# Kernel tuning notes

Measured on AMD Instinct MI355X. Metric: run time of the kernel, lower is better.

The kernel has to match this reference:

```python
import jax, jax.numpy as jnp
import numpy as np

D_MODEL, D_HEAD, N_HEADS, D_LATENT, D_ROPE = 2048, 128, 16, 512, 64
ROPE_BASE = 10000.0
SCALE = 1.0 / np.sqrt(D_HEAD + D_ROPE)


def _rope(x):
    # x: [B, H, T, d_rope]; GPT-NeoX style half-split rotary
    T, d = x.shape[-2], x.shape[-1]
    inv_freq = 1.0 / (ROPE_BASE ** (jnp.arange(0, d, 2, dtype=jnp.float32) / d))
    ang = jnp.arange(T, dtype=jnp.float32)[:, None] * inv_freq[None, :]  # [T, d/2]
    cos = jnp.concatenate([jnp.cos(ang), jnp.cos(ang)], axis=-1)  # [T, d]
    sin = jnp.concatenate([jnp.sin(ang), jnp.sin(ang)], axis=-1)
    x1, x2 = x[..., : d // 2], x[..., d // 2 :]
    rot = jnp.concatenate([-x2, x1], axis=-1)
    return x * cos + rot * sin


def setup_inputs() -> dict:
    key = jax.random.key(0)
    ks = jax.random.split(key, 8)
    B, T = 2, 2048
    s = 0.02
    inp = {
        "x": jax.random.normal(ks[0], (B, T, D_MODEL), jnp.float32),
        "w_q": jax.random.normal(ks[1], (D_MODEL, D_MODEL), jnp.float32) * s,
        "w_dkv": jax.random.normal(ks[2], (D_LATENT, D_MODEL), jnp.float32) * s,
        "w_ukv": jax.random.normal(ks[3], (2 * D_MODEL, D_LATENT), jnp.float32) * s,
        "w_o": jax.random.normal(ks[4], (D_MODEL, D_MODEL), jnp.float32) * s,
        "w_q_rot": jax.random.normal(ks[5], (N_HEADS * D_ROPE, D_MODEL), jnp.float32) * s,
        "w_k_rot": jax.random.normal(ks[6], (D_ROPE, D_MODEL), jnp.float32) * s,
        "mask": jnp.triu(jnp.ones((T, T), dtype=bool), 1),  # True = blocked (causal)
    }
    return inp


def reference(x, w_q, w_dkv, w_ukv, w_o, w_q_rot, w_k_rot, mask):
    B, T, _ = x.shape
    # content queries  [B, H, T, d_head]
    q = (x @ w_q.T).reshape(B, T, N_HEADS, D_HEAD).transpose(0, 2, 1, 3)
    # latent KV compression -> expansion
    dkv = x @ w_dkv.T                       # [B, T, d_latent]
    ukv = (dkv @ w_ukv.T).reshape(B, T, N_HEADS, 2 * D_HEAD).transpose(0, 2, 1, 3)
    k, v = ukv[..., :D_HEAD], ukv[..., D_HEAD:]
    # decoupled rope parts
    q_rot = (x @ w_q_rot.T).reshape(B, T, N_HEADS, D_ROPE).transpose(0, 2, 1, 3)
    k_rot = jnp.broadcast_to((x @ w_k_rot.T)[:, None, :, :], (B, N_HEADS, T, D_ROPE))
    q = jnp.concatenate([q, _rope(q_rot)], axis=-1)   # [B, H, T, d_head+d_rope]
    k = jnp.concatenate([k, _rope(k_rot)], axis=-1)
    # SDPA with True-means-blocked mask
    scores = jnp.einsum("bhqd,bhkd->bhqk", q, k) * SCALE
    scores = jnp.where(mask, -jnp.inf, scores)
    attn = jax.nn.softmax(scores, axis=-1)
    out = jnp.einsum("bhqk,bhkd->bhqd", attn, v)      # [B, H, T, d_head]
    out = out.transpose(0, 2, 1, 3).reshape(B, T, D_MODEL)
    return out @ w_o.T
```

## Files before the change

### kernel.cpp

```cpp
#include <hip/hip_runtime.h>
#include <hip/hip_bf16.h>
#include <math.h>

#define T_SEQ 2048
#define QSTR  3648

typedef __bf16 bf16x8 __attribute__((ext_vector_type(8)));
typedef float  f32x4  __attribute__((ext_vector_type(4)));
typedef float  f32x16 __attribute__((ext_vector_type(16)));
typedef unsigned int u32x4 __attribute__((ext_vector_type(4)));

#define GLOAD_LDS16(g, l) __builtin_amdgcn_global_load_lds( \
    (const __attribute__((address_space(1))) void*)(g),      \
    (__attribute__((address_space(3))) void*)(l), 16, 0, 0)

#define VMCNT(n) asm volatile("s_waitcnt vmcnt(" #n ")" ::: "memory")

static __device__ __forceinline__ unsigned cvtpk_bf16(float a, float b)
{
    unsigned r;
    asm("v_cvt_pk_bf16_f32 %0, %1, %2" : "=v"(r) : "v"(a), "v"(b));
    return r;
}

struct CastArgs {
    const float* s[7];
    __bf16*      d[7];
    unsigned     cum[8];
};

__global__ __launch_bounds__(256) void cast_all(CastArgs a)
{
    const unsigned blk = blockIdx.x;
    int idx = 0;
    #pragma unroll
    for (int i = 1; i < 7; i++) if (blk >= a.cum[i]) idx = i;
    const unsigned local = blk - a.cum[idx];
    const float* src = a.s[idx];
    __bf16* dst = a.d[idx];
    const int i = (int)(local * 256 + threadIdx.x) * 8;
    float4 va = *reinterpret_cast<const float4*>(src + i);
    float4 vb = *reinterpret_cast<const float4*>(src + i + 4);
    bf16x8 f;
    f[0] = (__bf16)va.x; f[1] = (__bf16)va.y; f[2] = (__bf16)va.z; f[3] = (__bf16)va.w;
    f[4] = (__bf16)vb.x; f[5] = (__bf16)vb.y; f[6] = (__bf16)vb.z; f[7] = (__bf16)vb.w;
    *reinterpret_cast<bf16x8*>(dst + i) = f;
}

__global__ __launch_bounds__(256) void rope_ip(__bf16* buf, int shift, int stride,
                                               int total)
{
    int gid = blockIdx.x * 256 + threadIdx.x;
    if (gid >= total) return;
    int row = gid >> shift;
    int rem = gid & ((1 << shift) - 1);
    int hb = rem >> 5, j = rem & 31;
    int t = row & (T_SEQ - 1);
    const float L2B = 0.4152410118609203f;
    float freq = exp2f(-L2B * (float)j);
    float sn, cs;
    __sincosf((float)t * freq, &sn, &cs);
    size_t base = (size_t)row * stride + hb * 64 + j;
    float v1 = (float)buf[base], v2 = (float)buf[base + 32];
    buf[base]      = (__bf16)(v1 * cs - v2 * sn);
    buf[base + 32] = (__bf16)(v2 * cs + v1 * sn);
}

__global__ __launch_bounds__(256) void prep_v(const __bf16* __restrict__ ukv,
                                              __bf16* __restrict__ vtt)
{
    __shared__ __align__(16) __bf16 Ls[64 * 136];
    const int tid = threadIdx.x;
    const int u = blockIdx.x, bh = blockIdx.y;
    const int b = bh >> 4, h = bh & 15;
    const size_t base = (size_t)b * T_SEQ + u * 64;
    #pragma unroll
    for (int p = 0; p < 4; p++) {
        int c = tid + 256 * p;
        int k = c >> 4, dv8 = (c & 15) * 8;
        *reinterpret_cast<bf16x8*>(Ls + k * 136 + dv8) =
            *reinterpret_cast<const bf16x8*>(ukv + (base + k) * 4096 + h * 256 + 128 + dv8);
    }
    __syncthreads();
    #pragma unroll
    for (int p = 0; p < 4; p++) {
        int c = tid + 256 * p;
        int dv = c >> 3, kb = c & 7;
        bf16x8 f;
        #pragma unroll
        for (int i = 0; i < 8; i++) f[i] = Ls[(kb * 8 + i) * 136 + dv];
        *reinterpret_cast<bf16x8*>(vtt + (((size_t)bh * 32 + u) * 128 + dv) * 64
                                   + ((kb ^ (dv & 7)) << 3)) = f;
    }
}

template <typename OutT>
__global__ __launch_bounds__(512, 2) void gemm_bt_256(const __bf16* __restrict__ A,
                                                      int lda,
                                                      const __bf16* __restrict__ B,
                                                      OutT* __restrict__ C,
                                                      int M, int N, int K)
{
    __shared__ __align__(16) __bf16 S[2 * 32768];
    const int tid  = threadIdx.x;
    const int lane = tid & 63;
    const int w    = tid >> 6;
    const int l15  = lane & 15, quad = lane >> 4;
    const int wm = w >> 2, wn = w & 3;
    const int m0 = blockIdx.y * 256, n0 = blockIdx.x * 256;
    const int NT = K >> 6;

    f32x4 acc[8][4] = {};
    bf16x8 af[4][2], bfr[2][2];

    auto stageA = [&](int T1, int h) {
        int d = T1 & 1;
        #pragma unroll
        for (int i = 0; i < 2; i++) {
            int c = i * 512 + tid;
            int lr = c >> 3, seg = c & 7;
            int g = ((lr >> 6) << 7) + h * 64 + (lr & 63);
            GLOAD_LDS16(A + (size_t)(m0 + g) * lda + T1 * 64 + ((seg ^ (lr & 7)) << 3),
                        S + d * 32768 + h * 8192 + c * 8);
        }
    };
    auto stageB = [&](int T1, int h) {
        int d = T1 & 1;
        #pragma unroll
        for (int i = 0; i < 2; i++) {
            int c = i * 512 + tid;
            int lr = c >> 3, seg = c & 7;
            int g = n0 + ((lr >> 5) << 6) + h * 32 + (lr & 31);
            if (g >= N) g = N - 1;
            GLOAD_LDS16(B + (size_t)g * K + T1 * 64 + ((seg ^ (lr & 7)) << 3),
                        S + d * 32768 + 16384 + h * 8192 + c * 8);
        }
    };

#define LOADA(d, mh) do {                                                      \
    const __bf16* Ah_ = S + (d) * 32768 + (mh) * 8192;                         \
    _Pragma("unroll")                                                          \
    for (int mi = 0; mi < 4; mi++) {                                           \
        int lr = wm * 64 + mi * 16 + l15;                                      \
        _Pragma("unroll")                                                      \
        for (int kk = 0; kk < 2; kk++)                                         \
            af[mi][kk] = *reinterpret_cast<const bf16x8*>(                     \
                Ah_ + lr * 64 + (((kk * 4 + quad) ^ (lr & 7)) << 3));          \
    }                                                                          \
} while (0)

#define LOADB(d, nh) do {                                                      \
    const __bf16* Bh_ = S + (d) * 32768 + 16384 + (nh) * 8192;                 \
    _Pragma("unroll")                                                          \
    for (int ni = 0; ni < 2; ni++) {                                           \
        int lr = wn * 32 + ni * 16 + l15;                                      \
        _Pragma("unroll")                                                      \
        for (int kk = 0; kk < 2; kk++)                                         \
            bfr[ni][kk] = *reinterpret_cast<const bf16x8*>(                    \
                Bh_ + lr * 64 + (((kk * 4 + quad) ^ (lr & 7)) << 3));          \
    }                                                                          \
} while (0)

#define SEAL() do {                                                            \
    __builtin_amdgcn_s_barrier();                                              \
    asm volatile("s_waitcnt lgkmcnt(0)" ::: "memory");                         \
    __builtin_amdgcn_sched_barrier(0);                                         \
} while (0)

#define MMA(mh, nh) do {                                                       \
    __builtin_amdgcn_s_setprio(1);                                             \
    _Pragma("unroll")                                                          \
    for (int mi = 0; mi < 4; mi++)                                             \
        _Pragma("unroll")                                                      \
        for (int ni = 0; ni < 2; ni++)                                         \
            _Pragma("unroll")                                                  \
            for (int kk = 0; kk < 2; kk++)                                     \
                acc[(mh) * 4 + mi][(nh) * 2 + ni] =                            \
                    __builtin_amdgcn_mfma_f32_16x16x32_bf16(                   \
                        af[mi][kk], bfr[ni][kk],                               \
                        acc[(mh) * 4 + mi][(nh) * 2 + ni], 0, 0, 0);           \
    __builtin_amdgcn_s_setprio(0);                                             \
} while (0)

    stageA(0, 0); stageB(0, 0); stageB(0, 1); stageA(0, 1);
    VMCNT(4);
    __builtin_amdgcn_s_barrier();

    for (int T = 0; T < NT - 1; T++) {
        const int d = T & 1;
        LOADA(d, 0); LOADB(d, 0); stageA(T + 1, 0); VMCNT(4); SEAL(); MMA(0, 0);
        LOADB(d, 1);              stageB(T + 1, 0); VMCNT(4); SEAL(); MMA(0, 1);
        LOADA(d, 1);              stageB(T + 1, 1);           SEAL(); MMA(1, 1);
        LOADB(d, 0);              stageA(T + 1, 1); VMCNT(4); SEAL(); MMA(1, 0);
    }
    {
        const int d = (NT - 1) & 1;
        LOADA(d, 0); LOADB(d, 0); VMCNT(2); SEAL(); MMA(0, 0);
        LOADB(d, 1);              VMCNT(0); SEAL(); MMA(0, 1);
        LOADA(d, 1);                        SEAL(); MMA(1, 1);
        LOADB(d, 0);                        SEAL(); MMA(1, 0);
    }
#undef LOADA
#undef LOADB
#undef SEAL
#undef MMA

    #pragma unroll
    for (int ai = 0; ai < 8; ai++) {
        #pragma unroll
        for (int bj = 0; bj < 4; bj++) {
            int col = n0 + wn * 64 + bj * 16 + l15;
            if (col < N) {
                #pragma unroll
                for (int r = 0; r < 4; r++) {
                    size_t row = m0 + wm * 128 + ai * 16 + quad * 4 + r;
                    C[row * (size_t)N + col] = (OutT)acc[ai][bj][r];
                }
            }
        }
    }
}

template <typename OutT>
__global__ __launch_bounds__(512) void gemm_bt_8ph(const __bf16* __restrict__ A,
                                                   int lda,
                                                   const __bf16* __restrict__ B,
                                                   OutT* __restrict__ C,
                                                   int M, int N, int K)
{
    __shared__ __align__(16) __bf16 S[2 * 24576];
    const int tid  = threadIdx.x;
    const int lane = tid & 63;
    const int w    = tid >> 6;
    const int l15  = lane & 15, quad = lane >> 4;
    const int wm = w >> 2, wn = w & 3;
    const int m0 = blockIdx.y * 128, n0 = blockIdx.x * 256;
    const int NT = K >> 6;

    f32x4 acc[4][4] = {};

    const int lrA = tid >> 3, segA = tid & 7;

    auto stageA = [&](int T1, int h) {
        int d = T1 & 1;
        int g = ((lrA >> 5) << 6) + h * 32 + (lrA & 31);
        GLOAD_LDS16(A + (size_t)(m0 + g) * lda + T1 * 64 + ((segA ^ (lrA & 7)) << 3),
                    S + d * 24576 + h * 4096 + tid * 8);
    };
    auto stageB = [&](int T1, int h) {
        int d = T1 & 1;
        #pragma unroll
        for (int i = 0; i < 2; i++) {
            int c = i * 512 + tid;
            int lr = c >> 3, seg = c & 7;
            int g = n0 + ((lr >> 5) << 6) + h * 32 + (lr & 31);
            if (g >= N) g = N - 1;
            GLOAD_LDS16(B + (size_t)g * K + T1 * 64 + ((seg ^ (lr & 7)) << 3),
                        S + d * 24576 + 8192 + h * 8192 + c * 8);
        }
    };

#define PHASE(d, mh, nh, STAGE, WAIT) do {                                     \
    const __bf16* Ah_ = S + (d) * 24576 + (mh) * 4096;                         \
    const __bf16* Bh_ = S + (d) * 24576 + 8192 + (nh) * 8192;                  \
    bf16x8 af[2][2], bfr[2][2];                                                \
    _Pragma("unroll")                                                          \
    for (int mr = 0; mr < 2; mr++) {                                           \
        int ar = wm * 32 + mr * 16 + l15;                                      \
        _Pragma("unroll")                                                      \
        for (int kk = 0; kk < 2; kk++)                                         \
            af[mr][kk] = *reinterpret_cast<const bf16x8*>(                     \
                Ah_ + ar * 64 + (((kk * 4 + quad) ^ (ar & 7)) << 3));          \
    }                                                                          \
    _Pragma("unroll")                                                          \
    for (int nr = 0; nr < 2; nr++) {                                           \
        int br = wn * 32 + nr * 16 + l15;                                      \
        _Pragma("unroll")                                                      \
        for (int kk = 0; kk < 2; kk++)                                         \
            bfr[nr][kk] = *reinterpret_cast<const bf16x8*>(                    \
                Bh_ + br * 64 + (((kk * 4 + quad) ^ (br & 7)) << 3));          \
    }                                                                          \
    STAGE;                                                                     \
    WAIT;                                                                      \
    __builtin_amdgcn_s_barrier();                                              \
    asm volatile("s_waitcnt lgkmcnt(0)" ::: "memory");                         \
    __builtin_amdgcn_sched_barrier(0);                                         \
    __builtin_amdgcn_s_setprio(1);                                             \
    _Pragma("unroll")                                                          \
    for (int mr = 0; mr < 2; mr++)                                             \
        _Pragma("unroll")                                                      \
        for (int nr = 0; nr < 2; nr++)                                         \
            _Pragma("unroll")                                                  \
            for (int kk = 0; kk < 2; kk++)                                     \
                acc[(mh) * 2 + mr][(nh) * 2 + nr] =                            \
                    __builtin_amdgcn_mfma_f32_16x16x32_bf16(                   \
                        af[mr][kk], bfr[nr][kk],                               \
                        acc[(mh) * 2 + mr][(nh) * 2 + nr], 0, 0, 0);           \
    __builtin_amdgcn_s_setprio(0);                                             \
} while (0)

    stageA(0, 0);
    stageB(0, 0);
    stageB(0, 1);
    stageA(0, 1);
    VMCNT(3);
    __builtin_amdgcn_s_barrier();

    for (int T = 0; T < NT - 1; T++) {
        const int d = T & 1;
        PHASE(d, 0, 0, stageA(T + 1, 0), VMCNT(2));
        PHASE(d, 0, 1, stageB(T + 1, 0), VMCNT(3));
        PHASE(d, 1, 0, stageB(T + 1, 1), (void)0);
        PHASE(d, 1, 1, stageA(T + 1, 1), VMCNT(3));
    }
    {
        const int d = (NT - 1) & 1;
        PHASE(d, 0, 0, (void)0, VMCNT(1));
        PHASE(d, 0, 1, (void)0, VMCNT(0));
        PHASE(d, 1, 0, (void)0, (void)0);
        PHASE(d, 1, 1, (void)0, (void)0);
    }
#undef PHASE

    #pragma unroll
    for (int ai = 0; ai < 4; ai++) {
        #pragma unroll
        for (int bj = 0; bj < 4; bj++) {
            int col = n0 + wn * 64 + bj * 16 + l15;
            if (col < N) {
                #pragma unroll
                for (int r = 0; r < 4; r++) {
                    size_t row = m0 + wm * 64 + ai * 16 + quad * 4 + r;
                    C[row * (size_t)N + col] = (OutT)acc[ai][bj][r];
                }
            }
        }
    }
}

__global__ __launch_bounds__(256, 2) void flash_mfma(
    const __bf16* __restrict__ qcat, const __bf16* __restrict__ ukv,
    const __bf16* __restrict__ vtt, __bf16* __restrict__ obuf)
{
    __shared__ __align__(16) __bf16 LDS[40960];

    const int tid  = threadIdx.x;
    const int w    = tid >> 6;
    const int lane = tid & 63;
    const int l31  = lane & 31;
    const int lh   = lane >> 5;
    const int l15  = lane & 15;
    const int quad = lane >> 4;
    const int gx = blockIdx.x, gy = blockIdx.y;
    int bh, qi;
    if (gy < 16) { bh = gy * 2;            qi = gx; }
    else         { bh = (gy - 16) * 2 + 1; qi = 15 - gx; }
    const int b = bh >> 4, h = bh & 15;
    const int q0 = qi * 128;
    const float SCALE = 0.07216878364870323f;
    const size_t urow = (size_t)b * T_SEQ;

    const int q = q0 + 32 * w + l31;
    bf16x8 qf[12];
    {
        const __bf16* qrow = qcat + (urow + q) * QSTR + h * 128;
        #pragma unroll
        for (int dk = 0; dk < 8; dk++)
            qf[dk] = *reinterpret_cast<const bf16x8*>(qrow + 16 * dk + 8 * lh);
        const __bf16* qrr = qcat + (urow + q) * QSTR + 2048 + h * 64;
        #pragma unroll
        for (int dk = 0; dk < 4; dk++)
            qf[8 + dk] = *reinterpret_cast<const bf16x8*>(qrr + 16 * dk + 8 * lh);
    }

    f32x16 o[4] = {};
    float m_i = -INFINITY, l_i = 0.f;

    const int nunits = 2 * qi + 2;

    auto stage = [&](int x) {
        const int d1 = x & 1;
        const size_t roff = urow + (size_t)64 * x;
        #pragma unroll
        for (int p = 0; p < 4; p++) {
            int c = tid + 256 * p;
            int row = c >> 4, seg = c & 15;
            GLOAD_LDS16(ukv + (roff + row) * 4096 + h * 256 + ((seg ^ (row & 7)) << 3),
                        LDS + d1 * 8192 + c * 8);
        }
        #pragma unroll
        for (int p = 0; p < 2; p++) {
            int c = tid + 256 * p;
            int row = c >> 3, seg = c & 7;
            GLOAD_LDS16(qcat + (roff + row) * QSTR + 3072 + ((seg ^ (row & 7)) << 3),
                        LDS + 16384 + d1 * 4096 + c * 8);
        }
        const __bf16* vsrc = vtt + ((size_t)bh * 32 + x) * 8192;
        #pragma unroll
        for (int p = 0; p < 4; p++) {
            int c = tid + 256 * p;
            GLOAD_LDS16(vsrc + c * 8, LDS + 24576 + d1 * 8192 + c * 8);
        }
    };

    stage(0);
    VMCNT(0);
    __builtin_amdgcn_s_barrier();

    for (int u = 0; u < nunits; u++) {
        if (u + 1 < nunits) { stage(u + 1); VMCNT(10); }
        else                { VMCNT(0); }
        __builtin_amdgcn_s_barrier();
        __builtin_amdgcn_sched_barrier(0);

        const int d1 = u & 1;
        const __bf16* KN = LDS + d1 * 8192;
        const __bf16* KR = LDS + 16384 + d1 * 4096;
        const __bf16* VT = LDS + 24576 + d1 * 8192;
        const int key = l31 & 7;

        f32x16 s2[2] = {};
        __builtin_amdgcn_s_setprio(1);
        #pragma unroll
        for (int t = 0; t < 2; t++) {
            const __bf16* kn = KN + (32 * t + l31) * 128;
            const __bf16* kr = KR + (32 * t + l31) * 64;
            #pragma unroll
            for (int dk = 0; dk < 8; dk++) {
                bf16x8 kf = *reinterpret_cast<const bf16x8*>(kn + (((2 * dk + lh) ^ key) << 3));
                s2[t] = __builtin_amdgcn_mfma_f32_32x32x16_bf16(kf, qf[dk], s2[t], 0, 0, 0);
            }
            #pragma unroll
            for (int dk = 0; dk < 4; dk++) {
                bf16x8 kf = *reinterpret_cast<const bf16x8*>(kr + (((2 * dk + lh) ^ key) << 3));
                s2[t] = __builtin_amdgcn_mfma_f32_32x32x16_bf16(kf, qf[8 + dk], s2[t], 0, 0, 0);
            }
        }
        __builtin_amdgcn_s_setprio(0);

        const int k0 = 64 * u;
        const bool domask = (u + 2 >= nunits);
        float rmax = -INFINITY;
        #pragma unroll
        for (int t = 0; t < 2; t++)
            #pragma unroll
            for (int g = 0; g < 16; g++) {
                float v = s2[t][g] * SCALE;
                if (domask) {
                    int kg = k0 + 32 * t + (g & 3) + 8 * (g >> 2) + 4 * lh;
                    if (kg > q) v = -INFINITY;
                }
                s2[t][g] = v;
                rmax = fmaxf(rmax, v);
            }
        rmax = fmaxf(rmax, __shfl_xor(rmax, 32, 64));
        const float mnew  = fmaxf(m_i, rmax);
        const float alpha = __expf(m_i - mnew);
        m_i = mnew;
        float part = 0.f;
        #pragma unroll
        for (int t = 0; t < 2; t++)
            #pragma unroll
            for (int g = 0; g < 16; g++) {
                float pv = __expf(s2[t][g] - mnew);
                s2[t][g] = pv;
                part += pv;
            }
        l_i = l_i * alpha + part;
        #pragma unroll
        for (int dt = 0; dt < 4; dt++) o[dt] *= alpha;

        __builtin_amdgcn_s_setprio(1);
        #pragma unroll
        for (int t = 0; t < 2; t++) {
            unsigned Ap[4], Bp[4];
            #pragma unroll
            for (int g = 0; g < 4; g++) {
                Ap[g] = cvtpk_bf16(s2[t][4 * g],     s2[t][4 * g + 1]);
                Bp[g] = cvtpk_bf16(s2[t][4 * g + 2], s2[t][4 * g + 3]);
            }
            #pragma unroll
            for (int sub = 0; sub < 2; sub++) {
                unsigned xA = lh ? Ap[2 * sub] : Ap[2 * sub + 1];
                unsigned xB = lh ? Bp[2 * sub] : Bp[2 * sub + 1];
                unsigned rA = __shfl_xor(xA, 32, 64);
                unsigned rB = __shfl_xor(xB, 32, 64);
                u32x4 uv;
                uv[0] = lh ? rA : Ap[2 * sub];
                uv[1] = lh ? rB : Bp[2 * sub];
                uv[2] = lh ? Ap[2 * sub + 1] : rA;
                uv[3] = lh ? Bp[2 * sub + 1] : rB;
                bf16x8 pf = __builtin_bit_cast(bf16x8, uv);
                const int s = 2 * t + sub;
                #pragma unroll
                for (int dt = 0; dt < 4; dt++) {
                    bf16x8 vf = *reinterpret_cast<const bf16x8*>(
                        VT + (32 * dt + l31) * 64 + (((2 * s + lh) ^ key) << 3));
                    o[dt] = __builtin_amdgcn_mfma_f32_32x32x16_bf16(vf, pf, o[dt], 0, 0, 0);
                }
            }
        }
        __builtin_amdgcn_s_setprio(0);

        __builtin_amdgcn_sched_barrier(0);
        __builtin_amdgcn_s_barrier();
    }

    const float linv = 1.0f / (l_i + __shfl_xor(l_i, 32, 64));
    float* Os = reinterpret_cast<float*>(LDS);
    #pragma unroll
    for (int dt = 0; dt < 4; dt++)
        #pragma unroll
        for (int g = 0; g < 16; g++) {
            int d = 32 * dt + (g & 3) + 8 * (g >> 2) + 4 * lh;
            Os[(32 * w + l31) * 132 + d] = o[dt][g] * linv;
        }
    asm volatile("s_waitcnt lgkmcnt(0)" ::: "memory");
    __builtin_amdgcn_sched_barrier(0);
    #pragma unroll
    for (int p = 0; p < 8; p++) {
        int row = 32 * w + 4 * p + quad;
        float4 a  = *reinterpret_cast<const float4*>(Os + row * 132 + 8 * l15);
        float4 c2 = *reinterpret_cast<const float4*>(Os + row * 132 + 8 * l15 + 4);
        bf16x8 f;
        f[0] = (__bf16)a.x;  f[1] = (__bf16)a.y;  f[2] = (__bf16)a.z;  f[3] = (__bf16)a.w;
        f[4] = (__bf16)c2.x; f[5] = (__bf16)c2.y; f[6] = (__bf16)c2.z; f[7] = (__bf16)c2.w;
        *reinterpret_cast<bf16x8*>(obuf + (urow + q0 + row) * 2048 + h * 128 + 8 * l15) = f;
    }
}

extern "C" void kernel_launch(void* const* d_in, const int* in_sizes, int n_in,
                              void* d_out, int out_size, void* d_ws, size_t ws_size,
                              hipStream_t stream)
{
    const float* x      = (const float*)d_in[0];
    const float* w_q    = (const float*)d_in[1];
    const float* w_dkv  = (const float*)d_in[2];
    const float* w_ukv  = (const float*)d_in[3];
    const float* w_o    = (const float*)d_in[4];
    const float* w_qrot = (const float*)d_in[5];
    const float* w_krot = (const float*)d_in[6];
    float* out = (float*)d_out;

    const size_t M = 4096;
    __bf16* ws   = (__bf16*)d_ws;
    __bf16* xb   = ws;
    __bf16* wcat = xb + M * 2048;
    __bf16* wqb  = wcat;
    __bf16* wqrb = wcat + (size_t)2048 * 2048;
    __bf16* wkrb = wqrb + (size_t)1024 * 2048;
    __bf16* wdkb = wkrb + (size_t)64 * 2048;
    __bf16* wukb = wcat + (size_t)QSTR * 2048;
    __bf16* wob  = wukb + (size_t)4096 * 512;
    __bf16* qcat = wob  + (size_t)2048 * 2048;
    __bf16* ukv  = qcat + M * QSTR;
    __bf16* ao   = ukv  + M * 4096;
    __bf16* vtt  = ao   + M * 2048;

    dim3 blk(256);

    CastArgs ca;
    ca.s[0] = x;      ca.d[0] = xb;
    ca.s[1] = w_q;    ca.d[1] = wqb;
    ca.s[2] = w_qrot; ca.d[2] = wqrb;
    ca.s[3] = w_krot; ca.d[3] = wkrb;
    ca.s[4] = w_dkv;  ca.d[4] = wdkb;
    ca.s[5] = w_ukv;  ca.d[5] = wukb;
    ca.s[6] = w_o;    ca.d[6] = wob;
    ca.cum[0] = 0;
    ca.cum[1] = ca.cum[0] + 4096;
    ca.cum[2] = ca.cum[1] + 2048;
    ca.cum[3] = ca.cum[2] + 1024;
    ca.cum[4] = ca.cum[3] + 64;
    ca.cum[5] = ca.cum[4] + 512;
    ca.cum[6] = ca.cum[5] + 1024;
    ca.cum[7] = ca.cum[6] + 2048;
    cast_all<<<ca.cum[7], blk, 0, stream>>>(ca);

    gemm_bt_256<__bf16><<<dim3(15, 16), dim3(512), 0, stream>>>(
        xb, 2048, wcat, qcat, 4096, QSTR, 2048);
    gemm_bt_256<__bf16><<<dim3(16, 16), dim3(512), 0, stream>>>(
        qcat + 3136, QSTR, wukb, ukv, 4096, 4096, 512);

    rope_ip<<<8192, blk, 0, stream>>>(qcat + 2048, 9, QSTR, 4096 * 512);
    rope_ip<<<512,  blk, 0, stream>>>(qcat + 3072, 5, QSTR, 4096 * 32);
    prep_v<<<dim3(32, 32), blk, 0, stream>>>(ukv, vtt);

    flash_mfma<<<dim3(16, 32), blk, 0, stream>>>(qcat, ukv, vtt, ao);

    gemm_bt_8ph<float><<<dim3(8, 32), dim3(512), 0, stream>>>(
        ao, 2048, wob, out, 4096, 2048, 2048);
}
```

Baseline: 370.0 us.

## Shrink flash attention tiles to 64 queries with 16x16x32 MFMA, single-buffered

```diff
diff --git a/kernel.cpp b/kernel.cpp
--- a/kernel.cpp
+++ b/kernel.cpp
@@ -7,7 +7,6 @@
 
 typedef __bf16 bf16x8 __attribute__((ext_vector_type(8)));
 typedef float  f32x4  __attribute__((ext_vector_type(4)));
-typedef float  f32x16 __attribute__((ext_vector_type(16)));
 typedef unsigned int u32x4 __attribute__((ext_vector_type(4)));
 
 #define GLOAD_LDS16(g, l) __builtin_amdgcn_global_load_lds( \
@@ -338,166 +337,153 @@
     }
 }
 
-__global__ __launch_bounds__(256, 2) void flash_mfma(
+__global__ __launch_bounds__(256, 4) void flash_mfma(
     const __bf16* __restrict__ qcat, const __bf16* __restrict__ ukv,
     const __bf16* __restrict__ vtt, __bf16* __restrict__ obuf)
 {
-    __shared__ __align__(16) __bf16 LDS[40960];
+    __shared__ __align__(16) __bf16 LDS[20480];
 
     const int tid  = threadIdx.x;
     const int w    = tid >> 6;
     const int lane = tid & 63;
-    const int l31  = lane & 31;
-    const int lh   = lane >> 5;
     const int l15  = lane & 15;
     const int quad = lane >> 4;
     const int gx = blockIdx.x, gy = blockIdx.y;
-    int bh, qi;
-    if (gy < 16) { bh = gy * 2;            qi = gx; }
-    else         { bh = (gy - 16) * 2 + 1; qi = 15 - gx; }
+    int bh, j;
+    if (gy < 16) { bh = gy * 2;            j = gx; }
+    else         { bh = (gy - 16) * 2 + 1; j = 31 - gx; }
     const int b = bh >> 4, h = bh & 15;
-    const int q0 = qi * 128;
+    const int q0 = j * 64;
     const float SCALE = 0.07216878364870323f;
     const size_t urow = (size_t)b * T_SEQ;
 
-    const int q = q0 + 32 * w + l31;
-    bf16x8 qf[12];
+    __bf16* KN = LDS;
+    __bf16* KR = LDS + 8192;
+    __bf16* VT = LDS + 12288;
+
+    const int q = q0 + 16 * w + l15;
+    bf16x8 qf[6];
     {
         const __bf16* qrow = qcat + (urow + q) * QSTR + h * 128;
         #pragma unroll
-        for (int dk = 0; dk < 8; dk++)
-            qf[dk] = *reinterpret_cast<const bf16x8*>(qrow + 16 * dk + 8 * lh);
+        for (int dkc = 0; dkc < 4; dkc++)
+            qf[dkc] = *reinterpret_cast<const bf16x8*>(qrow + 32 * dkc + 8 * quad);
         const __bf16* qrr = qcat + (urow + q) * QSTR + 2048 + h * 64;
-        #pragma unroll
-        for (int dk = 0; dk < 4; dk++)
-            qf[8 + dk] = *reinterpret_cast<const bf16x8*>(qrr + 16 * dk + 8 * lh);
-    }
-
-    f32x16 o[4] = {};
+        qf[4] = *reinterpret_cast<const bf16x8*>(qrr + 8 * quad);
+        qf[5] = *reinterpret_cast<const bf16x8*>(qrr + 32 + 8 * quad);
+    }
+
+    f32x4 o[8] = {};
     float m_i = -INFINITY, l_i = 0.f;
-
-    const int nunits = 2 * qi + 2;
-
-    auto stage = [&](int x) {
-        const int d1 = x & 1;
-        const size_t roff = urow + (size_t)64 * x;
+    const int key = l15 & 7;
+
+    auto stage = [&](int u) {
+        const size_t roff = urow + (size_t)64 * u;
         #pragma unroll
         for (int p = 0; p < 4; p++) {
             int c = tid + 256 * p;
             int row = c >> 4, seg = c & 15;
             GLOAD_LDS16(ukv + (roff + row) * 4096 + h * 256 + ((seg ^ (row & 7)) << 3),
-                        LDS + d1 * 8192 + c * 8);
+                        KN + c * 8);
         }
         #pragma unroll
         for (int p = 0; p < 2; p++) {
             int c = tid + 256 * p;
             int row = c >> 3, seg = c & 7;
             GLOAD_LDS16(qcat + (roff + row) * QSTR + 3072 + ((seg ^ (row & 7)) << 3),
-                        LDS + 16384 + d1 * 4096 + c * 8);
-        }
-        const __bf16* vsrc = vtt + ((size_t)bh * 32 + x) * 8192;
+                        KR + c * 8);
+        }
+        const __bf16* vsrc = vtt + ((size_t)bh * 32 + u) * 8192;
         #pragma unroll
         for (int p = 0; p < 4; p++) {
             int c = tid + 256 * p;
-            GLOAD_LDS16(vsrc + c * 8, LDS + 24576 + d1 * 8192 + c * 8);
+            GLOAD_LDS16(vsrc + c * 8, VT + c * 8);
         }
     };
 
-    stage(0);
-    VMCNT(0);
-    __builtin_amdgcn_s_barrier();
-
+    const int nunits = j + 1;
     for (int u = 0; u < nunits; u++) {
-        if (u + 1 < nunits) { stage(u + 1); VMCNT(10); }
-        else                { VMCNT(0); }
+        stage(u);
+        VMCNT(0);
         __builtin_amdgcn_s_barrier();
         __builtin_amdgcn_sched_barrier(0);
 
-        const int d1 = u & 1;
-        const __bf16* KN = LDS + d1 * 8192;
-        const __bf16* KR = LDS + 16384 + d1 * 4096;
-        const __bf16* VT = LDS + 24576 + d1 * 8192;
-        const int key = l31 & 7;
-
-        f32x16 s2[2] = {};
+        f32x4 s[4] = {};
         __builtin_amdgcn_s_setprio(1);
         #pragma unroll
-        for (int t = 0; t < 2; t++) {
-            const __bf16* kn = KN + (32 * t + l31) * 128;
-            const __bf16* kr = KR + (32 * t + l31) * 64;
+        for (int kt = 0; kt < 4; kt++) {
+            const __bf16* kn = KN + (16 * kt + l15) * 128;
+            const __bf16* kr = KR + (16 * kt + l15) * 64;
             #pragma unroll
-            for (int dk = 0; dk < 8; dk++) {
-                bf16x8 kf = *reinterpret_cast<const bf16x8*>(kn + (((2 * dk + lh) ^ key) << 3));
-                s2[t] = __builtin_amdgcn_mfma_f32_32x32x16_bf16(kf, qf[dk], s2[t], 0, 0, 0);
+            for (int dkc = 0; dkc < 4; dkc++) {
+                bf16x8 kf = *reinterpret_cast<const bf16x8*>(
+                    kn + (((4 * dkc + quad) ^ key) << 3));
+                s[kt] = __builtin_amdgcn_mfma_f32_16x16x32_bf16(kf, qf[dkc], s[kt], 0, 0, 0);
             }
             #pragma unroll
-            for (int dk = 0; dk < 4; dk++) {
-                bf16x8 kf = *reinterpret_cast<const bf16x8*>(kr + (((2 * dk + lh) ^ key) << 3));
-                s2[t] = __builtin_amdgcn_mfma_f32_32x32x16_bf16(kf, qf[8 + dk], s2[t], 0, 0, 0);
+            for (int dkc = 0; dkc < 2; dkc++) {
+                bf16x8 kf = *reinterpret_cast<const bf16x8*>(
+                    kr + (((4 * dkc + quad) ^ key) << 3));
+                s[kt] = __builtin_amdgcn_mfma_f32_16x16x32_bf16(kf, qf[4 + dkc], s[kt], 0, 0, 0);
             }
         }
         __builtin_amdgcn_s_setprio(0);
 
+        const bool domask = (u + 1 == nunits);
         const int k0 = 64 * u;
-        const bool domask = (u + 2 >= nunits);
         float rmax = -INFINITY;
         #pragma unroll
-        for (int t = 0; t < 2; t++)
+        for (int kt = 0; kt < 4; kt++)
             #pragma unroll
-            for (int g = 0; g < 16; g++) {
-                float v = s2[t][g] * SCALE;
-                if (domask) {
-                    int kg = k0 + 32 * t + (g & 3) + 8 * (g >> 2) + 4 * lh;
-                    if (kg > q) v = -INFINITY;
-                }
-                s2[t][g] = v;
+            for (int r = 0; r < 4; r++) {
+                float v = s[kt][r] * SCALE;
+                if (domask && (k0 + 16 * kt + 4 * quad + r > q)) v = -INFINITY;
+                s[kt][r] = v;
                 rmax = fmaxf(rmax, v);
             }
+        rmax = fmaxf(rmax, __shfl_xor(rmax, 16, 64));
         rmax = fmaxf(rmax, __shfl_xor(rmax, 32, 64));
         const float mnew  = fmaxf(m_i, rmax);
         const float alpha = __expf(m_i - mnew);
         m_i = mnew;
         float part = 0.f;
         #pragma unroll
-        for (int t = 0; t < 2; t++)
+        for (int kt = 0; kt < 4; kt++)
             #pragma unroll
-            for (int g = 0; g < 16; g++) {
-                float pv = __expf(s2[t][g] - mnew);
-                s2[t][g] = pv;
+            for (int r = 0; r < 4; r++) {
+                float pv = __expf(s[kt][r] - mnew);
+                s[kt][r] = pv;
                 part += pv;
             }
         l_i = l_i * alpha + part;
         #pragma unroll
-        for (int dt = 0; dt < 4; dt++) o[dt] *= alpha;
+        for (int dt = 0; dt < 8; dt++) o[dt] *= alpha;
 
         __builtin_amdgcn_s_setprio(1);
-        #pragma unroll
-        for (int t = 0; t < 2; t++) {
-            unsigned Ap[4], Bp[4];
+        const int hi = quad >> 1;
+        const int sA = 32 * (quad & 1) + l15;
+        const int sB = sA + 16;
+        #pragma unroll
+        for (int ks = 0; ks < 2; ks++) {
+            unsigned x0 = cvtpk_bf16(s[2 * ks][0], s[2 * ks][1]);
+            unsigned x1 = cvtpk_bf16(s[2 * ks][2], s[2 * ks][3]);
+            unsigned y0 = cvtpk_bf16(s[2 * ks + 1][0], s[2 * ks + 1][1]);
+            unsigned y1 = cvtpk_bf16(s[2 * ks + 1][2], s[2 * ks + 1][3]);
+            unsigned u0x = __shfl(x0, sA, 64), u0y = __shfl(y0, sA, 64);
+            unsigned u1x = __shfl(x1, sA, 64), u1y = __shfl(y1, sA, 64);
+            unsigned u2x = __shfl(x0, sB, 64), u2y = __shfl(y0, sB, 64);
+            unsigned u3x = __shfl(x1, sB, 64), u3y = __shfl(y1, sB, 64);
+            u32x4 uv;
+            uv[0] = hi ? u0y : u0x;
+            uv[1] = hi ? u1y : u1x;
+            uv[2] = hi ? u2y : u2x;
+            uv[3] = hi ? u3y : u3x;
+            bf16x8 pf = __builtin_bit_cast(bf16x8, uv);
             #pragma unroll
-            for (int g = 0; g < 4; g++) {
-                Ap[g] = cvtpk_bf16(s2[t][4 * g],     s2[t][4 * g + 1]);
-                Bp[g] = cvtpk_bf16(s2[t][4 * g + 2], s2[t][4 * g + 3]);
-            }
-            #pragma unroll
-            for (int sub = 0; sub < 2; sub++) {
-                unsigned xA = lh ? Ap[2 * sub] : Ap[2 * sub + 1];
-                unsigned xB = lh ? Bp[2 * sub] : Bp[2 * sub + 1];
-                unsigned rA = __shfl_xor(xA, 32, 64);
-                unsigned rB = __shfl_xor(xB, 32, 64);
-                u32x4 uv;
-                uv[0] = lh ? rA : Ap[2 * sub];
-                uv[1] = lh ? rB : Bp[2 * sub];
-                uv[2] = lh ? Ap[2 * sub + 1] : rA;
-                uv[3] = lh ? Bp[2 * sub + 1] : rB;
-                bf16x8 pf = __builtin_bit_cast(bf16x8, uv);
-                const int s = 2 * t + sub;
-                #pragma unroll
-                for (int dt = 0; dt < 4; dt++) {
-                    bf16x8 vf = *reinterpret_cast<const bf16x8*>(
-                        VT + (32 * dt + l31) * 64 + (((2 * s + lh) ^ key) << 3));
-                    o[dt] = __builtin_amdgcn_mfma_f32_32x32x16_bf16(vf, pf, o[dt], 0, 0, 0);
-                }
+            for (int dt = 0; dt < 8; dt++) {
+                bf16x8 vf = *reinterpret_cast<const bf16x8*>(
+                    VT + (16 * dt + l15) * 64 + (((4 * ks + quad) ^ key) << 3));
+                o[dt] = __builtin_amdgcn_mfma_f32_16x16x32_bf16(vf, pf, o[dt], 0, 0, 0);
             }
         }
         __builtin_amdgcn_s_setprio(0);
@@ -506,24 +492,26 @@
         __builtin_amdgcn_s_barrier();
     }
 
-    const float linv = 1.0f / (l_i + __shfl_xor(l_i, 32, 64));
+    l_i += __shfl_xor(l_i, 16, 64);
+    l_i += __shfl_xor(l_i, 32, 64);
+    const float linv = 1.0f / l_i;
     float* Os = reinterpret_cast<float*>(LDS);
     #pragma unroll
-    for (int dt = 0; dt < 4; dt++)
-        #pragma unroll
-        for (int g = 0; g < 16; g++) {
-            int d = 32 * dt + (g & 3) + 8 * (g >> 2) + 4 * lh;
-            Os[(32 * w + l31) * 132 + d] = o[dt][g] * linv;
+    for (int dt = 0; dt < 8; dt++)
+        #pragma unroll
+        for (int r = 0; r < 4; r++) {
+            int d = 16 * dt + 4 * quad + r;
+            Os[(16 * w + l15) * 132 + d] = o[dt][r] * linv;
         }
     asm volatile("s_waitcnt lgkmcnt(0)" ::: "memory");
     __builtin_amdgcn_sched_barrier(0);
     #pragma unroll
-    for (int p = 0; p < 8; p++) {
-        int row = 32 * w + 4 * p + quad;
-        float4 a  = *reinterpret_cast<const float4*>(Os + row * 132 + 8 * l15);
+    for (int p = 0; p < 4; p++) {
+        int row = 16 * w + 4 * p + quad;
+        float4 a4 = *reinterpret_cast<const float4*>(Os + row * 132 + 8 * l15);
         float4 c2 = *reinterpret_cast<const float4*>(Os + row * 132 + 8 * l15 + 4);
         bf16x8 f;
-        f[0] = (__bf16)a.x;  f[1] = (__bf16)a.y;  f[2] = (__bf16)a.z;  f[3] = (__bf16)a.w;
+        f[0] = (__bf16)a4.x; f[1] = (__bf16)a4.y; f[2] = (__bf16)a4.z; f[3] = (__bf16)a4.w;
         f[4] = (__bf16)c2.x; f[5] = (__bf16)c2.y; f[6] = (__bf16)c2.z; f[7] = (__bf16)c2.w;
         *reinterpret_cast<bf16x8*>(obuf + (urow + q0 + row) * 2048 + h * 128 + 8 * l15) = f;
     }
@@ -586,7 +574,7 @@
     rope_ip<<<512,  blk, 0, stream>>>(qcat + 3072, 5, QSTR, 4096 * 32);
     prep_v<<<dim3(32, 32), blk, 0, stream>>>(ukv, vtt);
 
-    flash_mfma<<<dim3(16, 32), blk, 0, stream>>>(qcat, ukv, vtt, ao);
+    flash_mfma<<<dim3(32, 32), blk, 0, stream>>>(qcat, ukv, vtt, ao);
 
     gemm_bt_8ph<float><<<dim3(8, 32), dim3(512), 0, stream>>>(
         ao, 2048, wob, out, 4096, 2048, 2048);
```

Result: slower. 384.4 us (+3.9%).
